# Kernel optimization log

Hardware: AMD Instinct MI355X
Metric: run time of the kernel (lower is better)

## Reference

```python
import jax, jax.numpy as jnp
import numpy as np

E = 8          # number of routed experts
TOP_K = 2      # experts per token
D = 2048       # hidden size
DFF = 1408     # per-expert intermediate
DFF_S = 2816   # shared-expert intermediate (2 shared experts fused)
B, S = 2, 2048


def setup_inputs() -> dict:
    key = jax.random.key(0)
    ks = jax.random.split(key, 8)
    sc = 0.02
    return {
        "hidden_states": jax.random.normal(ks[0], (B, S, D), jnp.float32),
        "gate_weight": jax.random.normal(ks[1], (E, D), jnp.float32) * sc,
        "w_gate": jax.random.normal(ks[2], (E, DFF, D), jnp.float32) * sc,
        "w_up": jax.random.normal(ks[3], (E, DFF, D), jnp.float32) * sc,
        "w_down": jax.random.normal(ks[4], (E, D, DFF), jnp.float32) * sc,
        "w_shared_gate": jax.random.normal(ks[5], (DFF_S, D), jnp.float32) * sc,
        "w_shared_up": jax.random.normal(ks[6], (DFF_S, D), jnp.float32) * sc,
        "w_shared_down": jax.random.normal(ks[7], (D, DFF_S), jnp.float32) * sc,
    }


def reference(hidden_states, gate_weight, w_gate, w_up, w_down,
              w_shared_gate, w_shared_up, w_shared_down):
    orig_shape = hidden_states.shape
    x = hidden_states.reshape(-1, orig_shape[-1])      # [T, D]

    # --- router (computed under no_grad in the original) ---
    logits = x @ gate_weight.T                          # [T, E]
    scores = jax.nn.softmax(logits, axis=-1)
    topk_w, topk_idx = jax.lax.top_k(scores, TOP_K)     # [T, K]
    topk_w = topk_w / jnp.sum(topk_w, axis=-1, keepdims=True)
    topk_w = jax.lax.stop_gradient(topk_w)
    topk_idx = jax.lax.stop_gradient(topk_idx)

    # dense combine weights [T, E] (equivalent to the masked per-expert loop +
    # weighted sum over the top-k copies)
    combine = jnp.einsum('tk,tke->te', topk_w,
                         jax.nn.one_hot(topk_idx, E, dtype=x.dtype))

    # --- routed experts: SwiGLU MLP per expert, dense over E ---
    g = jnp.einsum('td,efd->etf', x, w_gate)            # [E, T, DFF]
    u = jnp.einsum('td,efd->etf', x, w_up)
    h = jax.nn.silu(g) * u
    expert_out = jnp.einsum('etf,edf->etd', h, w_down)  # [E, T, D]
    y = jnp.einsum('etd,te->td', expert_out, combine)   # [T, D]

    # --- shared experts on the identity ---
    sh = jax.nn.silu(x @ w_shared_gate.T) * (x @ w_shared_up.T)
    y = y + sh @ w_shared_down.T

    return y.reshape(orig_shape)
```

## Files before the change

kernel.cpp:

```cpp
#include <hip/hip_runtime.h>
#include <stdint.h>
#include <stdio.h>

#define T_TOK 4096
#define DMODEL 2048
#define NEXP 8
#define DFF 1408
#define DFFS 2816
#define NSLOT 8192

#define GU_GRID (16 * 22 + 39 * 11)
#define DN_GRID (16 * 8 + 39 * 8)

typedef unsigned short u16;
typedef short s16x8 __attribute__((ext_vector_type(8)));
typedef unsigned short u16x4 __attribute__((ext_vector_type(4)));
typedef __bf16 bf16x8 __attribute__((ext_vector_type(8)));
typedef float f32x4 __attribute__((ext_vector_type(4)));

__device__ __forceinline__ u16 f2bf(float f) {
  uint32_t u = __builtin_bit_cast(uint32_t, f);
  u += 0x7fffu + ((u >> 16) & 1u);
  return (u16)(u >> 16);
}
__device__ __forceinline__ float bf2f(u16 h) {
  uint32_t u = ((uint32_t)h) << 16;
  return __builtin_bit_cast(float, u);
}

__device__ __forceinline__ void gl16(const u16* g, u16* l) {
  __builtin_amdgcn_global_load_lds((const __attribute__((address_space(1))) void*)g,
                                   (__attribute__((address_space(3))) void*)l,
                                   16, 0, 0);
}

#define BARRIER() asm volatile("s_barrier" ::: "memory")
#define SBAR()    __builtin_amdgcn_sched_barrier(0)

__global__ void k_convert6(const float* __restrict__ s0, u16* __restrict__ d0, int n0,
                           const float* __restrict__ s1, u16* __restrict__ d1, int n1,
                           const float* __restrict__ s2, u16* __restrict__ d2, int n2,
                           const float* __restrict__ s3, u16* __restrict__ d3, int n3,
                           const float* __restrict__ s4, u16* __restrict__ d4, int n4,
                           const float* __restrict__ s5, u16* __restrict__ d5, int n5) {
  int total = n0 + n1 + n2 + n3 + n4 + n5;
  int stride = gridDim.x * 256;
  for (int i = blockIdx.x * 256 + threadIdx.x; i < total; i += stride) {
    const float* s; u16* d; int k = i;
    if (k < n0) { s = s0; d = d0; }
    else { k -= n0;
      if (k < n1) { s = s1; d = d1; }
      else { k -= n1;
        if (k < n2) { s = s2; d = d2; }
        else { k -= n2;
          if (k < n3) { s = s3; d = d3; }
          else { k -= n3;
            if (k < n4) { s = s4; d = d4; }
            else { k -= n4; s = s5; d = d5; }
          }
        }
      }
    }
    float4 a = ((const float4*)s)[2 * k];
    float4 b = ((const float4*)s)[2 * k + 1];
    s16x8 r;
    r[0] = (short)f2bf(a.x); r[1] = (short)f2bf(a.y);
    r[2] = (short)f2bf(a.z); r[3] = (short)f2bf(a.w);
    r[4] = (short)f2bf(b.x); r[5] = (short)f2bf(b.y);
    r[6] = (short)f2bf(b.z); r[7] = (short)f2bf(b.w);
    ((s16x8*)d)[k] = r;
  }
}

__global__ void k_zero(int* __restrict__ counts) {
  if (threadIdx.x < NEXP) counts[threadIdx.x] = 0;
}

__global__ void k_router(const float* __restrict__ x, const float* __restrict__ gw,
                         u16* __restrict__ xb,
                         float* __restrict__ tkw, int* __restrict__ tki,
                         int* __restrict__ counts) {
  __shared__ double sm[NEXP];
  int t = blockIdx.x;
  int tid = threadIdx.x;
  int lane = tid & 63, wv = tid >> 6;
  const float4* xr = (const float4*)(x + (size_t)t * DMODEL);
  const float4* gr = (const float4*)gw;
  int e0 = wv * 2, e1 = e0 + 1;
  double a0 = 0.0, a1 = 0.0;
#pragma unroll
  for (int it = 0; it < DMODEL / 4 / 64; ++it) {
    int idx = it * 64 + lane;
    float4 xv = xr[idx];
    float4 g0 = gr[e0 * (DMODEL / 4) + idx];
    float4 g1 = gr[e1 * (DMODEL / 4) + idx];
    a0 += (double)xv.x * g0.x + (double)xv.y * g0.y +
          (double)xv.z * g0.z + (double)xv.w * g0.w;
    a1 += (double)xv.x * g1.x + (double)xv.y * g1.y +
          (double)xv.z * g1.z + (double)xv.w * g1.w;
    if (wv == 0) {
      u16x4 r = { f2bf(xv.x), f2bf(xv.y), f2bf(xv.z), f2bf(xv.w) };
      ((u16x4*)(xb + (size_t)t * DMODEL))[idx] = r;
    }
  }
#pragma unroll
  for (int off = 32; off; off >>= 1) {
    a0 += __shfl_down(a0, off, 64);
    a1 += __shfl_down(a1, off, 64);
  }
  if (lane == 0) { sm[e0] = a0; sm[e1] = a1; }
  __syncthreads();
  if (tid == 0) {
    double acc[NEXP];
#pragma unroll
    for (int e = 0; e < NEXP; ++e) acc[e] = sm[e];
    int i0 = 0; double v0 = acc[0];
    for (int e = 1; e < NEXP; ++e) if (acc[e] > v0) { v0 = acc[e]; i0 = e; }
    int i1 = -1; double v1 = -1e300;
    for (int e = 0; e < NEXP; ++e) if (e != i0 && acc[e] > v1) { v1 = acc[e]; i1 = e; }
    double r = exp(v1 - v0);
    float w0 = (float)(1.0 / (1.0 + r));
    float w1 = 1.0f - w0;
    tkw[2 * t] = w0; tkw[2 * t + 1] = w1;
    tki[2 * t] = i0; tki[2 * t + 1] = i1;
    atomicAdd(&counts[i0], 1);
    atomicAdd(&counts[i1], 1);
  }
}

__global__ void k_scan_sched(const int* __restrict__ counts, int* __restrict__ offs,
                             int* __restrict__ cursor, int* __restrict__ tblGU,
                             int* __restrict__ tblDN, int* __restrict__ nact) {
  if (threadIdx.x != 0 || blockIdx.x != 0) return;
  int s = 0;
  for (int e = 0; e < NEXP; ++e) { offs[e] = s; cursor[e] = s; s += counts[e]; }
  offs[NEXP] = s;
  int g = 0, d = 0;
  for (int m = 0; m < T_TOK / 256; ++m) {
    for (int nb = 0; nb < DFFS / 128; ++nb)
      tblGU[g++] = (int)(0x80000000u | (m << 12) | nb);
    for (int nb = 0; nb < DMODEL / 256; ++nb)
      tblDN[d++] = (int)(0x80000000u | (m << 12) | nb);
  }
  for (int e = 0; e < NEXP; ++e) {
    int mb = (counts[e] + 255) >> 8;
    for (int m = 0; m < mb; ++m) {
      for (int nb = 0; nb < DFF / 128; ++nb)
        tblGU[g++] = (e << 24) | (m << 12) | nb;
      for (int nb = 0; nb < DMODEL / 256; ++nb)
        tblDN[d++] = (e << 24) | (m << 12) | nb;
    }
  }
  nact[0] = g; nact[1] = d;
}

__global__ void k_assign(const int* __restrict__ tki, int* __restrict__ cursor,
                         int* __restrict__ pos, int* __restrict__ slot_tok) {
  int t = blockIdx.x * 256 + threadIdx.x;
  if (t >= T_TOK) return;
#pragma unroll
  for (int k = 0; k < 2; ++k) {
    int e = tki[2 * t + k];
    int p = atomicAdd(&cursor[e], 1);
    pos[2 * t + k] = p;
    slot_tok[p] = t;
  }
}

template <int PHASE>
__launch_bounds__(512, 2)
__global__ void k_gemm8(const int* __restrict__ tbl, const int* __restrict__ nact,
                        const u16* __restrict__ xb,
                        const u16* __restrict__ hr, const u16* __restrict__ hs,
                        const u16* __restrict__ wbg, const u16* __restrict__ wbu,
                        const u16* __restrict__ wbd,
                        const u16* __restrict__ wbsg, const u16* __restrict__ wbsu,
                        const u16* __restrict__ wbsd,
                        u16* __restrict__ P1r, u16* __restrict__ P1s,
                        u16* __restrict__ yr, float* __restrict__ out,
                        const int* __restrict__ offs, const int* __restrict__ counts,
                        const int* __restrict__ slot_tok) {
  __shared__ __attribute__((aligned(16))) u16 lds[2 * 32768];

  if ((int)blockIdx.x >= nact[PHASE]) return;
  const int desc = tbl[blockIdx.x];
  const bool shrd = desc < 0;
  const int e = (desc >> 24) & 0xF;
  const int m0 = ((desc >> 12) & 0xFFF) * 256;
  const int n0 = (desc & 0xFFF) * (PHASE == 0 ? 128 : 256);

  const u16 *A, *Bg, *Bu;
  u16* C1;
  float* OF = nullptr;
  int base, cnt, HS, K;
  bool gather = false;
  if constexpr (PHASE == 0) {
    K = DMODEL;
    if (shrd) {
      A = xb; base = 0; cnt = T_TOK;
      Bg = wbsg; Bu = wbsu; C1 = P1s; HS = DFFS;
    } else {
      A = xb; gather = true; base = offs[e]; cnt = counts[e];
      size_t es = (size_t)e * DFF * DMODEL;
      Bg = wbg + es; Bu = wbu + es; C1 = P1r; HS = DFF;
    }
  } else {
    HS = DMODEL;
    if (shrd) {
      A = hs; base = 0; cnt = T_TOK; K = DFFS;
      Bg = Bu = wbsd; OF = out; C1 = nullptr;
    } else {
      A = hr; base = offs[e]; cnt = counts[e]; K = DFF;
      Bg = Bu = wbd + (size_t)e * DMODEL * DFF; C1 = yr;
    }
  }
  const int NT = K >> 6;

  int tid = threadIdx.x;
  int lane = tid & 63, wv = tid >> 6;
  int wm = wv >> 2, wn = wv & 3;
  int fr = lane & 15, fq = lane >> 4;

  int srow = tid >> 3;
  int sslot = (tid & 7) ^ (srow & 7);
  const u16* ap[4]; const u16* bp[4];
#pragma unroll
  for (int h = 0; h < 4; ++h) {
    int r = h * 64 + srow;
    int ra = m0 + r; ra = ra < cnt ? ra : cnt - 1;
    int ga = gather ? slot_tok[base + ra] : base + ra;
    ap[h] = A + (size_t)ga * K + sslot * 8;
    const u16* bb;
    if constexpr (PHASE == 0) {
      int wnr = r >> 6, s = r & 63;
      int col = n0 + wnr * 32 + (s & 31);
      bb = (s < 32 ? Bg : Bu) + (size_t)col * K;
    } else {
      bb = Bg + (size_t)(n0 + r) * K;
    }
    bp[h] = bb + sslot * 8;
  }

#define STG_A(h, bufi, kt) gl16(ap[h] + (size_t)(kt) * 64, \
                                lds + (bufi) * 32768 + (h) * 4096 + wv * 512)
#define STG_B(h, bufi, kt) gl16(bp[h] + (size_t)(kt) * 64, \
                                lds + (bufi) * 32768 + 16384 + (h) * 4096 + wv * 512)

  int sKs0 = ((0 + fq) ^ (fr & 7)) * 8;
  int sKs1 = ((4 + fq) ^ (fr & 7)) * 8;
  int aBase = wm * 8192 + fr * 64;
  int bBase = 16384 + (wn >> 1) * 8192 + ((wn & 1) * 64 + fr) * 64;

  f32x4 acc[8][4];
#pragma unroll
  for (int i = 0; i < 8; ++i)
#pragma unroll
    for (int j = 0; j < 4; ++j) acc[i][j] = (f32x4){0.f, 0.f, 0.f, 0.f};

  STG_A(0, 0, 0); STG_A(1, 0, 0); STG_A(2, 0, 0); STG_A(3, 0, 0);
  STG_B(0, 0, 0); STG_B(1, 0, 0); STG_B(2, 0, 0); STG_B(3, 0, 0);
  if (NT > 1) { STG_A(0, 1, 1); STG_A(1, 1, 1); STG_A(2, 1, 1); STG_A(3, 1, 1); }
  if (NT > 1) asm volatile("s_waitcnt vmcnt(4)" ::: "memory");
  else        asm volatile("s_waitcnt vmcnt(0)" ::: "memory");
  BARRIER();
  SBAR();

  bf16x8 rAa[4][2], rAb[4][2], rB01[2][2], rB23[2][2];
#pragma unroll
  for (int il = 0; il < 4; ++il) {
    rAa[il][0] = *(const bf16x8*)(lds + aBase + il * 1024 + sKs0);
    rAa[il][1] = *(const bf16x8*)(lds + aBase + il * 1024 + sKs1);
  }
#pragma unroll
  for (int jl = 0; jl < 2; ++jl) {
    rB01[jl][0] = *(const bf16x8*)(lds + bBase + jl * 1024 + sKs0);
    rB01[jl][1] = *(const bf16x8*)(lds + bBase + jl * 1024 + sKs1);
  }

  for (int t = 0; t < NT; ++t) {
    const int buf = t & 1, nbuf = buf ^ 1;
    const u16* lbuf = lds + buf * 32768;
    const u16* lbufN = lds + nbuf * 32768;
    const bool hn1 = (t + 1) < NT, hn2 = (t + 2) < NT;

#pragma unroll
    for (int jl = 0; jl < 2; ++jl) {
      rB23[jl][0] = *(const bf16x8*)(lbuf + bBase + (2 + jl) * 1024 + sKs0);
      rB23[jl][1] = *(const bf16x8*)(lbuf + bBase + (2 + jl) * 1024 + sKs1);
    }
    if (hn1) { STG_B(0, nbuf, t + 1); STG_B(1, nbuf, t + 1); }
    __builtin_amdgcn_s_setprio(1);
#pragma unroll
    for (int il = 0; il < 4; ++il)
#pragma unroll
      for (int jl = 0; jl < 2; ++jl) {
        acc[il][jl] = __builtin_amdgcn_mfma_f32_16x16x32_bf16(rAa[il][0], rB01[jl][0], acc[il][jl], 0, 0, 0);
        acc[il][jl] = __builtin_amdgcn_mfma_f32_16x16x32_bf16(rAa[il][1], rB01[jl][1], acc[il][jl], 0, 0, 0);
      }
    __builtin_amdgcn_s_setprio(0);

#pragma unroll
    for (int il = 0; il < 4; ++il) {
      rAb[il][0] = *(const bf16x8*)(lbuf + aBase + (4 + il) * 1024 + sKs0);
      rAb[il][1] = *(const bf16x8*)(lbuf + aBase + (4 + il) * 1024 + sKs1);
    }
    if (hn1) { STG_B(2, nbuf, t + 1); STG_B(3, nbuf, t + 1); }
    __builtin_amdgcn_s_setprio(1);
#pragma unroll
    for (int il = 0; il < 4; ++il)
#pragma unroll
      for (int jl = 0; jl < 2; ++jl) {
        acc[il][2 + jl] = __builtin_amdgcn_mfma_f32_16x16x32_bf16(rAa[il][0], rB23[jl][0], acc[il][2 + jl], 0, 0, 0);
        acc[il][2 + jl] = __builtin_amdgcn_mfma_f32_16x16x32_bf16(rAa[il][1], rB23[jl][1], acc[il][2 + jl], 0, 0, 0);
      }
    __builtin_amdgcn_s_setprio(0);

    asm volatile("s_waitcnt lgkmcnt(0)" ::: "memory");
    BARRIER();
    SBAR();
    if (hn2) { STG_A(0, buf, t + 2); STG_A(1, buf, t + 2); }
    __builtin_amdgcn_s_setprio(1);
#pragma unroll
    for (int il = 0; il < 4; ++il)
#pragma unroll
      for (int jl = 0; jl < 2; ++jl) {
        acc[4 + il][jl] = __builtin_amdgcn_mfma_f32_16x16x32_bf16(rAb[il][0], rB01[jl][0], acc[4 + il][jl], 0, 0, 0);
        acc[4 + il][jl] = __builtin_amdgcn_mfma_f32_16x16x32_bf16(rAb[il][1], rB01[jl][1], acc[4 + il][jl], 0, 0, 0);
      }
    __builtin_amdgcn_s_setprio(0);

    if (hn1) {
      if (hn2) asm volatile("s_waitcnt vmcnt(2)" ::: "memory");
      else     asm volatile("s_waitcnt vmcnt(0)" ::: "memory");
      BARRIER();
      SBAR();
      if (hn2) { STG_A(2, buf, t + 2); STG_A(3, buf, t + 2); }
#pragma unroll
      for (int il = 0; il < 4; ++il) {
        rAa[il][0] = *(const bf16x8*)(lbufN + aBase + il * 1024 + sKs0);
        rAa[il][1] = *(const bf16x8*)(lbufN + aBase + il * 1024 + sKs1);
      }
#pragma unroll
      for (int jl = 0; jl < 2; ++jl) {
        rB01[jl][0] = *(const bf16x8*)(lbufN + bBase + jl * 1024 + sKs0);
        rB01[jl][1] = *(const bf16x8*)(lbufN + bBase + jl * 1024 + sKs1);
      }
    }
    __builtin_amdgcn_s_setprio(1);
#pragma unroll
    for (int il = 0; il < 4; ++il)
#pragma unroll
      for (int jl = 0; jl < 2; ++jl) {
        acc[4 + il][2 + jl] = __builtin_amdgcn_mfma_f32_16x16x32_bf16(rAb[il][0], rB23[jl][0], acc[4 + il][2 + jl], 0, 0, 0);
        acc[4 + il][2 + jl] = __builtin_amdgcn_mfma_f32_16x16x32_bf16(rAb[il][1], rB23[jl][1], acc[4 + il][2 + jl], 0, 0, 0);
      }
    __builtin_amdgcn_s_setprio(0);
  }
#undef STG_A
#undef STG_B

#pragma unroll
  for (int i = 0; i < 8; ++i) {
    int row_t = wm * 128 + i * 16 + fq * 4;
#pragma unroll
    for (int r = 0; r < 4; ++r) {
      int m = m0 + row_t + r;
      if (m >= cnt) continue;
      size_t rowoff = (size_t)(base + m) * (size_t)HS;
      if constexpr (PHASE == 0) {
#pragma unroll
        for (int jl = 0; jl < 2; ++jl) {
          float g = acc[i][jl][r];
          float u = acc[i][2 + jl][r];
          float hval = (g / (1.f + __expf(-g))) * u;
          C1[rowoff + (n0 + wn * 32 + jl * 16 + fr)] = f2bf(hval);
        }
      } else {
#pragma unroll
        for (int j = 0; j < 4; ++j) {
          int col_t = n0 + wn * 64 + j * 16 + fr;
          float v = acc[i][j][r];
          if (shrd) OF[rowoff + col_t] = v;
          else      C1[rowoff + col_t] = f2bf(v);
        }
      }
    }
  }
}

__global__ void k_combine(float* __restrict__ y, const u16* __restrict__ yr,
                          const float* __restrict__ tkw, const int* __restrict__ pos) {
  int t = blockIdx.x;
  int i = threadIdx.x;
  float w0 = tkw[2 * t], w1 = tkw[2 * t + 1];
  size_t p0 = (size_t)pos[2 * t] * DMODEL, p1 = (size_t)pos[2 * t + 1] * DMODEL;
  int d0 = i * 8;
  s16x8 a = *(const s16x8*)(yr + p0 + d0);
  s16x8 b = *(const s16x8*)(yr + p1 + d0);
  float* yo = y + (size_t)t * DMODEL + d0;
#pragma unroll
  for (int j = 0; j < 8; ++j)
    yo[j] += w0 * bf2f((u16)a[j]) + w1 * bf2f((u16)b[j]);
}

extern "C" void kernel_launch(void* const* d_in, const int* in_sizes, int n_in,
                              void* d_out, int out_size, void* d_ws, size_t ws_size,
                              hipStream_t stream) {
  const float* x   = (const float*)d_in[0];
  const float* gw  = (const float*)d_in[1];
  const float* wg  = (const float*)d_in[2];
  const float* wu  = (const float*)d_in[3];
  const float* wd  = (const float*)d_in[4];
  const float* wsg = (const float*)d_in[5];
  const float* wsu = (const float*)d_in[6];
  const float* wsd = (const float*)d_in[7];
  float* out = (float*)d_out;

  char* ws = (char*)d_ws;
  size_t o = 0;
  auto alloc = [&](size_t bytes) -> void* {
    void* p = ws + o;
    o += (bytes + 255) & ~(size_t)255;
    return p;
  };
  u16* xb   = (u16*)alloc((size_t)T_TOK * DMODEL * 2);
  u16* wbg  = (u16*)alloc((size_t)NEXP * DFF * DMODEL * 2);
  u16* wbu  = (u16*)alloc((size_t)NEXP * DFF * DMODEL * 2);
  u16* wbd  = (u16*)alloc((size_t)NEXP * DMODEL * DFF * 2);
  u16* wbsg = (u16*)alloc((size_t)DFFS * DMODEL * 2);
  u16* wbsu = (u16*)alloc((size_t)DFFS * DMODEL * 2);
  u16* wbsd = (u16*)alloc((size_t)DMODEL * DFFS * 2);
  u16* P1r  = (u16*)alloc((size_t)NSLOT * DFF * 2);
  u16* P1s  = (u16*)alloc((size_t)T_TOK * DFFS * 2);
  u16* yr   = (u16*)alloc((size_t)NSLOT * DMODEL * 2);
  float* tkw = (float*)alloc((size_t)T_TOK * 2 * 4);
  int* tki   = (int*)alloc((size_t)T_TOK * 2 * 4);
  int* pos   = (int*)alloc((size_t)T_TOK * 2 * 4);
  int* slot_tok = (int*)alloc((size_t)NSLOT * 4);
  int* counts   = (int*)alloc(64);
  int* offs     = (int*)alloc(64);
  int* cursor   = (int*)alloc(64);
  int* tblGU    = (int*)alloc(GU_GRID * 4);
  int* tblDN    = (int*)alloc(DN_GRID * 4);
  int* nact     = (int*)alloc(64);
  if (o > ws_size) {
    fprintf(stderr, "kernel_launch: ws too small: need %zu have %zu\n", o, ws_size);
    return;
  }

  {
    int n8w = NEXP * DFF * DMODEL / 8;
    int n8s = DFFS * DMODEL / 8;
    k_convert6<<<2048, 256, 0, stream>>>(wg, wbg, n8w, wu, wbu, n8w, wd, wbd, n8w,
                                         wsg, wbsg, n8s, wsu, wbsu, n8s, wsd, wbsd, n8s);
  }

  k_zero<<<1, 64, 0, stream>>>(counts);
  k_router<<<T_TOK, 256, 0, stream>>>(x, gw, xb, tkw, tki, counts);
  k_scan_sched<<<1, 64, 0, stream>>>(counts, offs, cursor, tblGU, tblDN, nact);
  k_assign<<<(T_TOK + 255) / 256, 256, 0, stream>>>(tki, cursor, pos, slot_tok);

  k_gemm8<0><<<GU_GRID, 512, 0, stream>>>(
      tblGU, nact, xb, nullptr, nullptr,
      wbg, wbu, wbd, wbsg, wbsu, wbsd,
      P1r, P1s, yr, out, offs, counts, slot_tok);

  k_gemm8<1><<<DN_GRID, 512, 0, stream>>>(
      tblDN, nact, xb, P1r, P1s,
      wbg, wbu, wbd, wbsg, wbsu, wbsd,
      P1r, P1s, yr, out, offs, counts, slot_tok);

  k_combine<<<T_TOK, 256, 0, stream>>>(out, yr, tkw, pos);
}
```

Baseline: 555.3 us.

## Group tiles sharing a weight column onto the same XCD via round-robin table

The scheduler now builds fixed-size tile tables interleaved by XCD (index pos*8+x), assigning all M-tiles of a given weight column block to the least-loaded of eight XCD queues, so tiles reusing the same weight slice share an L2. Empty slots are filled with a sentinel that makes those blocks exit early, and a bound check skips tiles beyond an expert's token count. This aims to cut redundant weight traffic across XCD L2 caches. The tradeoff is a fixed grid sized for a worst case, with more idle blocks and possible load imbalance if the greedy packing overflows its per-XCD capacity.

```diff
diff --git a/kernel.cpp b/kernel.cpp
--- a/kernel.cpp
+++ b/kernel.cpp
@@ -9,8 +9,11 @@
 #define DFFS 2816
 #define NSLOT 8192
 
-#define GU_GRID (16 * 22 + 39 * 11)
-#define DN_GRID (16 * 8 + 39 * 8)
+#define GU_PXL 120
+#define DN_PXL 96
+#define GU_GRID (8 * GU_PXL)
+#define DN_GRID (8 * DN_PXL)
+#define SENTINEL 0x7FFFFFFF
 
 typedef unsigned short u16;
 typedef short s16x8 __attribute__((ext_vector_type(8)));
@@ -135,23 +138,47 @@
   int s = 0;
   for (int e = 0; e < NEXP; ++e) { offs[e] = s; cursor[e] = s; s += counts[e]; }
   offs[NEXP] = s;
-  int g = 0, d = 0;
-  for (int m = 0; m < T_TOK / 256; ++m) {
-    for (int nb = 0; nb < DFFS / 128; ++nb)
-      tblGU[g++] = (int)(0x80000000u | (m << 12) | nb);
-    for (int nb = 0; nb < DMODEL / 256; ++nb)
-      tblDN[d++] = (int)(0x80000000u | (m << 12) | nb);
-  }
-  for (int e = 0; e < NEXP; ++e) {
-    int mb = (counts[e] + 255) >> 8;
-    for (int m = 0; m < mb; ++m) {
-      for (int nb = 0; nb < DFF / 128; ++nb)
-        tblGU[g++] = (e << 24) | (m << 12) | nb;
-      for (int nb = 0; nb < DMODEL / 256; ++nb)
-        tblDN[d++] = (e << 24) | (m << 12) | nb;
-    }
-  }
-  nact[0] = g; nact[1] = d;
+  for (int i = 0; i < GU_GRID; ++i) tblGU[i] = SENTINEL;
+  for (int i = 0; i < DN_GRID; ++i) tblDN[i] = SENTINEL;
+
+  int mb[NEXP];
+  for (int e = 0; e < NEXP; ++e) mb[e] = (counts[e] + 255) >> 8;
+
+  {
+    int load[8] = {0}, pos[8] = {0};
+    for (int nb = 0; nb < DFFS / 128; ++nb) {
+      int x = 0; for (int q = 1; q < 8; ++q) if (load[q] < load[x]) x = q;
+      for (int m = 0; m < T_TOK / 256; ++m)
+        tblGU[(pos[x]++) * 8 + x] = (int)(0x80000000u | (m << 12) | nb);
+      load[x] += T_TOK / 256;
+    }
+    for (int e = 0; e < NEXP; ++e)
+      for (int nb = 0; nb < DFF / 128; ++nb) {
+        if (mb[e] == 0) continue;
+        int x = 0; for (int q = 1; q < 8; ++q) if (load[q] < load[x]) x = q;
+        for (int m = 0; m < mb[e]; ++m)
+          tblGU[(pos[x]++) * 8 + x] = (e << 24) | (m << 12) | nb;
+        load[x] += mb[e];
+      }
+  }
+  {
+    int load[8] = {0}, pos[8] = {0};
+    for (int nb = 0; nb < DMODEL / 256; ++nb) {
+      int x = 0; for (int q = 1; q < 8; ++q) if (load[q] < load[x]) x = q;
+      for (int m = 0; m < T_TOK / 256; ++m)
+        tblDN[(pos[x]++) * 8 + x] = (int)(0x80000000u | (m << 12) | nb);
+      load[x] += 2 * (T_TOK / 256);
+    }
+    for (int e = 0; e < NEXP; ++e)
+      for (int nb = 0; nb < DMODEL / 256; ++nb) {
+        if (mb[e] == 0) continue;
+        int x = 0; for (int q = 1; q < 8; ++q) if (load[q] < load[x]) x = q;
+        for (int m = 0; m < mb[e]; ++m)
+          tblDN[(pos[x]++) * 8 + x] = (e << 24) | (m << 12) | nb;
+        load[x] += mb[e];
+      }
+  }
+  nact[0] = GU_GRID; nact[1] = DN_GRID;
 }
 
 __global__ void k_assign(const int* __restrict__ tki, int* __restrict__ cursor,
@@ -182,10 +209,10 @@
                         const int* __restrict__ slot_tok) {
   __shared__ __attribute__((aligned(16))) u16 lds[2 * 32768];
 
-  if ((int)blockIdx.x >= nact[PHASE]) return;
   const int desc = tbl[blockIdx.x];
+  const int e = (desc >> 24) & 0xF;
+  if (e == 0xF) return;
   const bool shrd = desc < 0;
-  const int e = (desc >> 24) & 0xF;
   const int m0 = ((desc >> 12) & 0xFFF) * 256;
   const int n0 = (desc & 0xFFF) * (PHASE == 0 ? 128 : 256);
 
@@ -214,6 +241,7 @@
       Bg = Bu = wbd + (size_t)e * DMODEL * DFF; C1 = yr;
     }
   }
+  if (m0 >= cnt) return;
   const int NT = K >> 6;
 
   int tid = threadIdx.x;
```

New measurement: 647.7 us. 1.17x slower.

## Fuse weight fp32-to-bf16 conversion into router and gate/up GEMM launches

Applied to the files above, without the earlier changes.

Removes the separate six-tensor conversion kernel. Gate/up and shared gate/up weights are now converted by extra blocks appended to the router launch. Down-projection weights are converted by extra blocks appended to the gate/up GEMM launch, so that conversion can overlap with GEMM work that does not need it. The aim is to hide conversion bandwidth behind other kernels and save a launch, at the cost of contention with the GEMM blocks and dependence on block scheduling order.

```diff
diff --git a/kernel.cpp b/kernel.cpp
--- a/kernel.cpp
+++ b/kernel.cpp
@@ -11,6 +11,8 @@
 
 #define GU_GRID (16 * 22 + 39 * 11)
 #define DN_GRID (16 * 8 + 39 * 8)
+#define CONV_GU 1024
+#define CONV_DN 512
 
 typedef unsigned short u16;
 typedef short s16x8 __attribute__((ext_vector_type(8)));
@@ -37,39 +39,16 @@
 #define BARRIER() asm volatile("s_barrier" ::: "memory")
 #define SBAR()    __builtin_amdgcn_sched_barrier(0)
 
-__global__ void k_convert6(const float* __restrict__ s0, u16* __restrict__ d0, int n0,
-                           const float* __restrict__ s1, u16* __restrict__ d1, int n1,
-                           const float* __restrict__ s2, u16* __restrict__ d2, int n2,
-                           const float* __restrict__ s3, u16* __restrict__ d3, int n3,
-                           const float* __restrict__ s4, u16* __restrict__ d4, int n4,
-                           const float* __restrict__ s5, u16* __restrict__ d5, int n5) {
-  int total = n0 + n1 + n2 + n3 + n4 + n5;
-  int stride = gridDim.x * 256;
-  for (int i = blockIdx.x * 256 + threadIdx.x; i < total; i += stride) {
-    const float* s; u16* d; int k = i;
-    if (k < n0) { s = s0; d = d0; }
-    else { k -= n0;
-      if (k < n1) { s = s1; d = d1; }
-      else { k -= n1;
-        if (k < n2) { s = s2; d = d2; }
-        else { k -= n2;
-          if (k < n3) { s = s3; d = d3; }
-          else { k -= n3;
-            if (k < n4) { s = s4; d = d4; }
-            else { k -= n4; s = s5; d = d5; }
-          }
-        }
-      }
-    }
-    float4 a = ((const float4*)s)[2 * k];
-    float4 b = ((const float4*)s)[2 * k + 1];
-    s16x8 r;
-    r[0] = (short)f2bf(a.x); r[1] = (short)f2bf(a.y);
-    r[2] = (short)f2bf(a.z); r[3] = (short)f2bf(a.w);
-    r[4] = (short)f2bf(b.x); r[5] = (short)f2bf(b.y);
-    r[6] = (short)f2bf(b.z); r[7] = (short)f2bf(b.w);
-    ((s16x8*)d)[k] = r;
-  }
+__device__ __forceinline__ void conv8(const float* __restrict__ s, u16* __restrict__ d,
+                                      long k) {
+  float4 a = ((const float4*)s)[2 * k];
+  float4 b = ((const float4*)s)[2 * k + 1];
+  s16x8 r;
+  r[0] = (short)f2bf(a.x); r[1] = (short)f2bf(a.y);
+  r[2] = (short)f2bf(a.z); r[3] = (short)f2bf(a.w);
+  r[4] = (short)f2bf(b.x); r[5] = (short)f2bf(b.y);
+  r[6] = (short)f2bf(b.z); r[7] = (short)f2bf(b.w);
+  ((s16x8*)d)[k] = r;
 }
 
 __global__ void k_zero(int* __restrict__ counts) {
@@ -79,7 +58,29 @@
 __global__ void k_router(const float* __restrict__ x, const float* __restrict__ gw,
                          u16* __restrict__ xb,
                          float* __restrict__ tkw, int* __restrict__ tki,
-                         int* __restrict__ counts) {
+                         int* __restrict__ counts,
+                         const float* __restrict__ wgF, u16* __restrict__ wbg,
+                         const float* __restrict__ wuF, u16* __restrict__ wbu,
+                         const float* __restrict__ wsgF, u16* __restrict__ wbsg,
+                         const float* __restrict__ wsuF, u16* __restrict__ wbsu) {
+  if (blockIdx.x >= T_TOK) {
+    const long N1 = (long)NEXP * DFF * DMODEL / 8;
+    const long NS = (long)DFFS * DMODEL / 8;
+    const long total = 2 * N1 + 2 * NS;
+    const long stride = (long)CONV_GU * 256;
+    for (long i = (long)(blockIdx.x - T_TOK) * 256 + threadIdx.x; i < total; i += stride) {
+      long k = i;
+      if (k < N1)            conv8(wgF, wbg, k);
+      else { k -= N1;
+        if (k < N1)          conv8(wuF, wbu, k);
+        else { k -= N1;
+          if (k < NS)        conv8(wsgF, wbsg, k);
+          else               conv8(wsuF, wbsu, k - NS);
+        }
+      }
+    }
+    return;
+  }
   __shared__ double sm[NEXP];
   int t = blockIdx.x;
   int tid = threadIdx.x;
@@ -176,12 +177,28 @@
                         const u16* __restrict__ wbd,
                         const u16* __restrict__ wbsg, const u16* __restrict__ wbsu,
                         const u16* __restrict__ wbsd,
+                        const float* __restrict__ wdF, const float* __restrict__ wsdF,
+                        u16* __restrict__ wbdW, u16* __restrict__ wbsdW,
                         u16* __restrict__ P1r, u16* __restrict__ P1s,
                         u16* __restrict__ yr, float* __restrict__ out,
                         const int* __restrict__ offs, const int* __restrict__ counts,
                         const int* __restrict__ slot_tok) {
   __shared__ __attribute__((aligned(16))) u16 lds[2 * 32768];
 
+  if constexpr (PHASE == 0) {
+    if ((int)blockIdx.x >= GU_GRID) {
+      const long N1 = (long)NEXP * DMODEL * DFF / 8;
+      const long NS = (long)DMODEL * DFFS / 8;
+      const long total = N1 + NS;
+      const long stride = (long)CONV_DN * 512;
+      for (long i = (long)(blockIdx.x - GU_GRID) * 512 + threadIdx.x; i < total;
+           i += stride) {
+        if (i < N1) conv8(wdF, wbdW, i);
+        else        conv8(wsdF, wbsdW, i - N1);
+      }
+      return;
+    }
+  }
   if ((int)blockIdx.x >= nact[PHASE]) return;
   const int desc = tbl[blockIdx.x];
   const bool shrd = desc < 0;
@@ -448,26 +465,22 @@
     return;
   }
 
-  {
-    int n8w = NEXP * DFF * DMODEL / 8;
-    int n8s = DFFS * DMODEL / 8;
-    k_convert6<<<2048, 256, 0, stream>>>(wg, wbg, n8w, wu, wbu, n8w, wd, wbd, n8w,
-                                         wsg, wbsg, n8s, wsu, wbsu, n8s, wsd, wbsd, n8s);
-  }
-
   k_zero<<<1, 64, 0, stream>>>(counts);
-  k_router<<<T_TOK, 256, 0, stream>>>(x, gw, xb, tkw, tki, counts);
+  k_router<<<T_TOK + CONV_GU, 256, 0, stream>>>(x, gw, xb, tkw, tki, counts,
+                                                wg, wbg, wu, wbu, wsg, wbsg, wsu, wbsu);
   k_scan_sched<<<1, 64, 0, stream>>>(counts, offs, cursor, tblGU, tblDN, nact);
   k_assign<<<(T_TOK + 255) / 256, 256, 0, stream>>>(tki, cursor, pos, slot_tok);
 
-  k_gemm8<0><<<GU_GRID, 512, 0, stream>>>(
+  k_gemm8<0><<<GU_GRID + CONV_DN, 512, 0, stream>>>(
       tblGU, nact, xb, nullptr, nullptr,
       wbg, wbu, wbd, wbsg, wbsu, wbsd,
+      wd, wsd, wbd, wbsd,
       P1r, P1s, yr, out, offs, counts, slot_tok);
 
   k_gemm8<1><<<DN_GRID, 512, 0, stream>>>(
       tblDN, nact, xb, P1r, P1s,
       wbg, wbu, wbd, wbsg, wbsu, wbsd,
+      nullptr, nullptr, nullptr, nullptr,
       P1r, P1s, yr, out, offs, counts, slot_tok);
 
   k_combine<<<T_TOK, 256, 0, stream>>>(out, yr, tkw, pos);
```

Measured after the change: 534.9 us. 1.04x faster.
